# Optimization experiments

Measured on AMD Instinct MI355X. Metric: run time of the kernel, lower is better.

## Reference

```python
import jax, jax.numpy as jnp
import numpy as np

B, L, D, H, DFF = 8, 1024, 256, 8, 2048
DH = D // H


def setup_inputs() -> dict:
    key = jax.random.key(0)
    ks = jax.random.split(key, 12)

    def w(k, shape):
        return jax.random.normal(k, shape, dtype=jnp.float32) * 0.02

    # continuous padding: first `length` tokens valid, rest padded (mask True = pad)
    lengths = jax.random.randint(ks[0], (B,), L // 4, L + 1)
    mask = jnp.arange(L)[None, :] >= lengths[:, None]

    return {
        "src": jax.random.normal(ks[1], (B, L, D), dtype=jnp.float32),
        "src_key_padding_mask": mask,
        "in_proj_w": w(ks[2], (3 * D, D)),
        "in_proj_b": w(ks[3], (3 * D,)),
        "out_w": w(ks[4], (D, D)),
        "out_b": w(ks[5], (D,)),
        "proj_w": w(ks[6], (D, D)),
        "proj_b": w(ks[7], (D,)),
        "ff1_w": w(ks[8], (DFF, D)),
        "ff1_b": w(ks[9], (DFF,)),
        "ff2_w": w(ks[10], (D, DFF)),
        "ff2_b": w(ks[11], (D,)),
    }


def reference(src, src_key_padding_mask, in_proj_w, in_proj_b, out_w, out_b,
              proj_w, proj_b, ff1_w, ff1_b, ff2_w, ff2_b):
    mask = src_key_padding_mask  # [B, L], True = padding
    neg_inf = jnp.float32(-jnp.inf)

    # --- make_attn_mask (vectorized, continuous padding) ---
    s = (~mask).sum(axis=1).astype(jnp.float32)              # [B] valid lengths
    idx = jnp.arange(L, dtype=jnp.float32)
    dist = jnp.abs(idx[:, None] - idx[None, :])              # [L, L]
    valid_tok = idx[None, :] < s[:, None]                    # [B, L]
    pair_ok = valid_tok[:, :, None] & valid_tok[:, None, :]  # [B, L, L]
    bias = jnp.where(pair_ok, (s[:, None, None] - dist[None]) / s[:, None, None], neg_inf)
    # rows that are entirely -inf (padded query rows) are zeroed, like masked_fill
    row_pad = ~valid_tok                                     # [B, L]
    bias = jnp.where(row_pad[:, :, None], 0.0, bias)
    # key_padding_mask is merged additively (as in nn.MultiheadAttention)
    add_mask = bias + jnp.where(mask[:, None, :], neg_inf, 0.0)  # [B, L, L]

    # --- multi-head self-attention ---
    qkv = src @ in_proj_w.T + in_proj_b                      # [B, L, 3D]
    q, k, v = jnp.split(qkv, 3, axis=-1)

    def heads(t):
        return t.reshape(B, L, H, DH).transpose(0, 2, 1, 3)  # [B, H, L, DH]

    q, k, v = heads(q), heads(k), heads(v)
    scale = 1.0 / jnp.sqrt(jnp.float32(DH))
    scores = jnp.einsum('bhqd,bhkd->bhqk', q, k) * scale + add_mask[:, None]
    attn = jax.nn.softmax(scores, axis=-1)
    ctx = jnp.einsum('bhqk,bhkd->bhqd', attn, v)
    ctx = ctx.transpose(0, 2, 1, 3).reshape(B, L, D)
    h_attn = ctx @ out_w.T + out_b

    # --- residual proj + FFN (no layernorm, no dropout) ---
    h = src + (h_attn @ proj_w.T + proj_b)
    ff = jax.nn.gelu(h @ ff1_w.T + ff1_b, approximate=False) @ ff2_w.T + ff2_b
    h = h + ff

    # zero out padded rows (masked_fill with all_neg_inf)
    h = jnp.where(row_pad[:, :, None], 0.0, h)
    return h
```

## Files before the change

### kernel.cpp

```cpp
#include <hip/hip_runtime.h>
#include <hip/hip_bf16.h>


#define BB   8
#define LL   1024
#define DD   256
#define HHN  8
#define DHH  32
#define DFFN 2048

typedef __attribute__((ext_vector_type(8))) __bf16 bf16x8;
typedef __attribute__((ext_vector_type(4))) float f32x4;

__device__ inline void gload16(const void* g, void* l) {
  __builtin_amdgcn_global_load_lds(
      (const __attribute__((address_space(1))) void*)g,
      (__attribute__((address_space(3))) void*)l, 16, 0, 0);
}

#define NCVT0 (BB * LL * DD)
#define NCVT1 (768 * DD)
#define NCVT2 (DFFN * DD)
#define NCVT3 (DD * DFFN)
#define NB_CVT ((NCVT0 + NCVT1 + NCVT2 + NCVT3) / 2048)

__global__ __launch_bounds__(256) void preamble_kernel(
    const float* __restrict__ src, const unsigned char* __restrict__ mb,
    const float* __restrict__ in_proj_w, const float* __restrict__ ff1_w,
    const float* __restrict__ ff2_w, const float* __restrict__ proj_w,
    const float* __restrict__ out_w, const float* __restrict__ proj_b,
    const float* __restrict__ out_b, __hip_bfloat16* __restrict__ src_bf,
    __hip_bfloat16* __restrict__ wqkv_bf, __hip_bfloat16* __restrict__ wff1_bf,
    __hip_bfloat16* __restrict__ wff2_bf, __hip_bfloat16* __restrict__ wc_bf,
    float* __restrict__ bc, int* __restrict__ lens) {
  const int bid = blockIdx.x;
  const int tid = threadIdx.x;
  __shared__ float red[256];
  __shared__ int cnt[BB];
  __shared__ int flag3f, flagNA;

  if (bid < NB_CVT) {
    int i = bid * 2048 + tid * 8;
    const float* s;
    __hip_bfloat16* d;
    if (i < NCVT0) { s = src; d = src_bf; }
    else if (i < NCVT0 + NCVT1) { s = in_proj_w; d = wqkv_bf; i -= NCVT0; }
    else if (i < NCVT0 + NCVT1 + NCVT2) { s = ff1_w; d = wff1_bf; i -= NCVT0 + NCVT1; }
    else { s = ff2_w; d = wff2_bf; i -= NCVT0 + NCVT1 + NCVT2; }
    const float4 a = *(const float4*)(s + i);
    const float4 b = *(const float4*)(s + i + 4);
    bf16x8 o;
    o[0] = (__bf16)a.x; o[1] = (__bf16)a.y; o[2] = (__bf16)a.z; o[3] = (__bf16)a.w;
    o[4] = (__bf16)b.x; o[5] = (__bf16)b.y; o[6] = (__bf16)b.z; o[7] = (__bf16)b.w;
    *(bf16x8*)(d + i) = o;
  } else if (bid == NB_CVT) {
    if (tid == 0) { flag3f = 0; flagNA = 0; }
    if (tid < BB) cnt[tid] = 0;
    __syncthreads();
    for (int i = tid; i < BB * LL; i += 256) {
      unsigned char v = mb[i];
      if (v) {
        if ((i & 3) == 3 && v == 0x3F) flag3f = 1;
        else if (i & 3) flagNA = 1;
      }
    }
    __syncthreads();
    const bool isfloat = (flag3f != 0);
    const bool isbool = (!isfloat) && (flagNA != 0);
    if (isbool) {
      for (int i = tid; i < BB * LL; i += 256)
        if (mb[i] == 0) atomicAdd(&cnt[i >> 10], 1);
    } else {
      const int* mi = (const int*)mb;
      for (int i = tid; i < BB * LL; i += 256)
        if (mi[i] == 0) atomicAdd(&cnt[i >> 10], 1);
    }
    __syncthreads();
    if (tid < BB) lens[tid] = cnt[tid];
  } else {
    const int i0 = (bid - NB_CVT - 1) << 2;
    const int k = tid;
    float acc[4] = {0.f, 0.f, 0.f, 0.f};
    for (int n = 0; n < DD; ++n) {
      const float won = out_w[n * DD + k];
#pragma unroll
      for (int j = 0; j < 4; ++j)
        acc[j] = fmaf(proj_w[(i0 + j) * DD + n], won, acc[j]);
    }
#pragma unroll
    for (int j = 0; j < 4; ++j) wc_bf[(i0 + j) * DD + k] = (__hip_bfloat16)acc[j];
#pragma unroll
    for (int j = 0; j < 4; ++j) {
      red[k] = proj_w[(i0 + j) * DD + k] * out_b[k];
      __syncthreads();
      for (int sft = 128; sft > 0; sft >>= 1) {
        if (k < sft) red[k] += red[k + sft];
        __syncthreads();
      }
      if (k == 0) bc[i0 + j] = proj_b[i0 + j] + red[0];
      __syncthreads();
    }
  }
}

template <int EPI, int BM>
__global__ __launch_bounds__(256) void gemm_bf16(
    const __hip_bfloat16* __restrict__ A, const __hip_bfloat16* __restrict__ W,
    const float* __restrict__ bias, const float* __restrict__ resid,
    float* __restrict__ Cf, __hip_bfloat16* __restrict__ Cb, const int M,
    const int N, const int K, const int* __restrict__ lens) {
  constexpr int MF = BM / 32;
  constexpr int CH = BM / 64;
  __shared__ __bf16 As[2][BM][32];
  __shared__ __bf16 Bs[2][128][32];

  const int tid = threadIdx.x;
  const int w = tid >> 6;
  const int lane = tid & 63;
  const int c = lane & 15;
  const int hq = lane >> 4;
  const int h8 = hq << 3;
  const int wr = w >> 1, wc = w & 1;
  const int c0 = blockIdx.x << 7;
  const int r0 = blockIdx.y * BM;

  const int mylen = lens[r0 >> 10];
  if ((r0 & (LL - 1)) >= mylen) return;

  const int srow = tid >> 2;
  const int scol = (tid & 3) << 3;

  auto STAGE = [&](int buf, int kt) {
    const int k0 = kt << 5;
#pragma unroll
    for (int ch = 0; ch < CH; ++ch)
      gload16(A + (size_t)(r0 + (ch << 6) + srow) * K + k0 + scol,
              &As[buf][(ch << 6) + (w << 4)][0]);
#pragma unroll
    for (int ch = 0; ch < 2; ++ch)
      gload16(W + (size_t)(c0 + (ch << 6) + srow) * K + k0 + scol,
              &Bs[buf][(ch << 6) + (w << 4)][0]);
  };

  f32x4 acc[MF][4];
#pragma unroll
  for (int m = 0; m < MF; ++m)
#pragma unroll
    for (int n = 0; n < 4; ++n) acc[m][n] = (f32x4){0.f, 0.f, 0.f, 0.f};

  const int nkt = K >> 5;
  int buf = 0;
  STAGE(0, 0);
  __syncthreads();
  for (int kt = 0; kt < nkt; ++kt) {
    if (kt + 1 < nkt) STAGE(buf ^ 1, kt + 1);
    bf16x8 af[MF], bfr[4];
#pragma unroll
    for (int m = 0; m < MF; ++m)
      af[m] = *(const bf16x8*)&As[buf][wr * (MF * 16) + (m << 4) + c][h8];
#pragma unroll
    for (int n = 0; n < 4; ++n)
      bfr[n] = *(const bf16x8*)&Bs[buf][(wc << 6) + (n << 4) + c][h8];
#pragma unroll
    for (int m = 0; m < MF; ++m)
#pragma unroll
      for (int n = 0; n < 4; ++n)
        acc[m][n] =
            __builtin_amdgcn_mfma_f32_16x16x32_bf16(af[m], bfr[n], acc[m][n], 0, 0, 0);
    __syncthreads();
    buf ^= 1;
  }

  float bv[4];
#pragma unroll
  for (int n = 0; n < 4; ++n) bv[n] = bias[c0 + (wc << 6) + (n << 4) + c];

#pragma unroll
  for (int m = 0; m < MF; ++m) {
#pragma unroll
    for (int i = 0; i < 4; ++i) {
      const int gr = r0 + wr * (MF * 16) + (m << 4) + (hq << 2) + i;
#pragma unroll
      for (int n = 0; n < 4; ++n) {
        const int gc = c0 + (wc << 6) + (n << 4) + c;
        float v = acc[m][n][i] + bv[n];
        if (EPI == 1) v = 0.5f * v * (1.0f + erff(v * 0.70710678118654752f));
        if (EPI == 2) {
          v += resid[(size_t)gr * N + gc];
          Cf[(size_t)gr * N + gc] = v;
        }
        Cb[(size_t)gr * N + gc] = (__hip_bfloat16)v;
      }
    }
  }
}

__global__ __launch_bounds__(256) void gemm_ff2_part(
    const __hip_bfloat16* __restrict__ A, const __hip_bfloat16* __restrict__ W,
    float* __restrict__ P, const int* __restrict__ lens) {
  constexpr int MF = 2;
  __shared__ __bf16 As[2][64][32];
  __shared__ __bf16 Bs[2][128][32];

  const int tid = threadIdx.x;
  const int w = tid >> 6;
  const int lane = tid & 63;
  const int c = lane & 15;
  const int hq = lane >> 4;
  const int h8 = hq << 3;
  const int wr = w >> 1, wc = w & 1;
  const int c0 = blockIdx.x << 7;
  const int r0 = blockIdx.y << 6;
  if ((r0 & (LL - 1)) >= lens[r0 >> 10]) return;

  const int kz = blockIdx.z;
  const int kbase = kz << 9;
  const int srow = tid >> 2;
  const int scol = (tid & 3) << 3;

  auto STAGE = [&](int buf, int kt) {
    const int k0 = kbase + (kt << 5);
    gload16(A + (size_t)(r0 + srow) * DFFN + k0 + scol, &As[buf][w << 4][0]);
#pragma unroll
    for (int ch = 0; ch < 2; ++ch)
      gload16(W + (size_t)(c0 + (ch << 6) + srow) * DFFN + k0 + scol,
              &Bs[buf][(ch << 6) + (w << 4)][0]);
  };

  f32x4 acc[MF][4];
#pragma unroll
  for (int m = 0; m < MF; ++m)
#pragma unroll
    for (int n = 0; n < 4; ++n) acc[m][n] = (f32x4){0.f, 0.f, 0.f, 0.f};

  int buf = 0;
  STAGE(0, 0);
  __syncthreads();
  for (int kt = 0; kt < 16; ++kt) {
    if (kt + 1 < 16) STAGE(buf ^ 1, kt + 1);
    bf16x8 af[MF], bfr[4];
#pragma unroll
    for (int m = 0; m < MF; ++m)
      af[m] = *(const bf16x8*)&As[buf][wr * (MF * 16) + (m << 4) + c][h8];
#pragma unroll
    for (int n = 0; n < 4; ++n)
      bfr[n] = *(const bf16x8*)&Bs[buf][(wc << 6) + (n << 4) + c][h8];
#pragma unroll
    for (int m = 0; m < MF; ++m)
#pragma unroll
      for (int n = 0; n < 4; ++n)
        acc[m][n] =
            __builtin_amdgcn_mfma_f32_16x16x32_bf16(af[m], bfr[n], acc[m][n], 0, 0, 0);
    __syncthreads();
    buf ^= 1;
  }

  float* Pz = P + (size_t)kz * (BB * LL) * DD;
#pragma unroll
  for (int m = 0; m < MF; ++m)
#pragma unroll
    for (int i = 0; i < 4; ++i) {
      const int gr = r0 + wr * (MF * 16) + (m << 4) + (hq << 2) + i;
#pragma unroll
      for (int n = 0; n < 4; ++n)
        Pz[(size_t)gr * DD + c0 + (wc << 6) + (n << 4) + c] = acc[m][n][i];
    }
}

__global__ __launch_bounds__(256) void ff2_reduce(
    const float* __restrict__ P, const float* __restrict__ resid,
    const float* __restrict__ bias, float* __restrict__ out,
    const int* __restrict__ lens) {
  const int idx = blockIdx.x * 256 + threadIdx.x;
  const int r = idx >> 6;
  const int c4 = (idx & 63) << 2;
  float4 o;
  if ((r & (LL - 1)) >= lens[r >> 10]) {
    o.x = o.y = o.z = o.w = 0.f;
  } else {
    const size_t base = (size_t)r * DD + c4;
    o = *(const float4*)&resid[base];
    const float4 bv = *(const float4*)&bias[c4];
    o.x += bv.x; o.y += bv.y; o.z += bv.z; o.w += bv.w;
#pragma unroll
    for (int z = 0; z < 4; ++z) {
      const float4 pv = *(const float4*)&P[(size_t)z * (BB * LL) * DD + base];
      o.x += pv.x; o.y += pv.y; o.z += pv.z; o.w += pv.w;
    }
  }
  *(float4*)&out[(size_t)r * DD + c4] = o;
}

__global__ __launch_bounds__(256) void attn_fwd_mfma(
    const __hip_bfloat16* __restrict__ qkv, __hip_bfloat16* __restrict__ ctx,
    const int* __restrict__ lens) {
  __shared__ __bf16 Ks[2][64][56];
  __shared__ __bf16 Vt[2][32][66];
  __shared__ __bf16 Pl[4][16][72];

  const int tid = threadIdx.x;
  const int q0 = blockIdx.x << 6;
  const int hh = blockIdx.y;
  const int b = blockIdx.z;
  const int slen = lens[b];
  if (q0 >= slen) return;

  const int w = tid >> 6;
  const int lane = tid & 63;
  const int c = lane & 15;
  const int h = lane >> 4;
  const int h8 = h << 3;

  const float L2E = 1.44269504f;
  const float sf = (float)slen;
  const float cb = -7.0f * L2E;
  const float cd = (1.0f / sf) * L2E;
  const float qscale = 0.17677669529663689f * L2E;

  bf16x8 qf;
  {
    const int qrow = q0 + (w << 4) + c;
    const bf16x8 qraw =
        *(const bf16x8*)(qkv + (size_t)(b * LL + qrow) * 768 + hh * DHH + h8);
#pragma unroll
    for (int j = 0; j < 8; ++j) qf[j] = (__bf16)((float)qraw[j] * qscale);
  }

  f32x4 acc0 = {0.f, 0.f, 0.f, 0.f};
  f32x4 acc1 = {0.f, 0.f, 0.f, 0.f};
  float lsum[4] = {0.f, 0.f, 0.f, 0.f};

  const int skey = tid >> 2;
  const int sdg = (tid & 3) << 3;
  const int ntk = (slen + 63) >> 6;
  const int qg = q0 + (w << 4) + (h << 2);

  const __hip_bfloat16* kvbase = qkv + (size_t)b * LL * 768 + 256 + hh * DHH + sdg;

  bf16x8 kreg, vreg;
  {
    const __hip_bfloat16* kb = kvbase + (size_t)skey * 768;
    kreg = *(const bf16x8*)kb;
    vreg = *(const bf16x8*)(kb + 256);
    *(bf16x8*)&Ks[0][skey][sdg] = kreg;
#pragma unroll
    for (int j = 0; j < 8; ++j) Vt[0][sdg + j][skey] = vreg[j];
  }
  if (ntk > 1) {
    const __hip_bfloat16* kb = kvbase + (size_t)(64 + skey) * 768;
    kreg = *(const bf16x8*)kb;
    vreg = *(const bf16x8*)(kb + 256);
  }
  __syncthreads();

  for (int kt = 0; kt < ntk; ++kt) {
    const int p = kt & 1;
    const int kbase = kt << 6;

    f32x4 st[4];
    __builtin_amdgcn_s_setprio(1);
#pragma unroll
    for (int t = 0; t < 4; ++t) {
      const bf16x8 kf = *(const bf16x8*)&Ks[p][(t << 4) + c][h8];
      st[t] = __builtin_amdgcn_mfma_f32_16x16x32_bf16(
          qf, kf, (f32x4){0.f, 0.f, 0.f, 0.f}, 0, 0, 0);
    }
    __builtin_amdgcn_s_setprio(0);

#pragma unroll
    for (int t = 0; t < 4; ++t) {
      const int kj = kbase + (t << 4) + c;
      const bool kvalid = kj < slen;
      const float kjf = (float)kj;
#pragma unroll
      for (int i = 0; i < 4; ++i) {
        const float dist = fabsf((float)(qg + i) - kjf);
        const float arg = kvalid ? (st[t][i] + cb - dist * cd) : -1e30f;
        const float pv = __builtin_amdgcn_exp2f(arg);
        lsum[i] += pv;
        Pl[w][(h << 2) + i][c + (t << 4)] = (__bf16)pv;
      }
    }

    asm volatile("s_waitcnt lgkmcnt(0)" ::: "memory");

    __builtin_amdgcn_s_setprio(1);
#pragma unroll
    for (int n = 0; n < 2; ++n) {
      const bf16x8 pf = *(const bf16x8*)&Pl[w][c][h8 + (n << 5)];
      const uint32_t* v0p = (const uint32_t*)&Vt[p][c][h8 + (n << 5)];
      const uint32_t* v1p = (const uint32_t*)&Vt[p][16 + c][h8 + (n << 5)];
      union { uint32_t u[4]; bf16x8 v; } t0, t1;
#pragma unroll
      for (int j = 0; j < 4; ++j) { t0.u[j] = v0p[j]; t1.u[j] = v1p[j]; }
      acc0 = __builtin_amdgcn_mfma_f32_16x16x32_bf16(pf, t0.v, acc0, 0, 0, 0);
      acc1 = __builtin_amdgcn_mfma_f32_16x16x32_bf16(pf, t1.v, acc1, 0, 0, 0);
    }
    __builtin_amdgcn_s_setprio(0);

    if (kt + 1 < ntk) {
      *(bf16x8*)&Ks[p ^ 1][skey][sdg] = kreg;
#pragma unroll
      for (int j = 0; j < 8; ++j) Vt[p ^ 1][sdg + j][skey] = vreg[j];
      if (kt + 2 < ntk) {
        const __hip_bfloat16* kb = kvbase + (size_t)(((kt + 2) << 6) + skey) * 768;
        kreg = *(const bf16x8*)kb;
        vreg = *(const bf16x8*)(kb + 256);
      }
    }
    __syncthreads();
  }

#pragma unroll
  for (int i = 0; i < 4; ++i) {
    float l = lsum[i];
    l += __shfl_xor(l, 1);
    l += __shfl_xor(l, 2);
    l += __shfl_xor(l, 4);
    l += __shfl_xor(l, 8);
    const float il = 1.0f / l;
    __hip_bfloat16* op =
        ctx + (size_t)(b * LL + q0 + (w << 4) + (h << 2) + i) * 256 + hh * DHH;
    op[c] = (__hip_bfloat16)(acc0[i] * il);
    op[c + 16] = (__hip_bfloat16)(acc1[i] * il);
  }
}

extern "C" void kernel_launch(void* const* d_in, const int* in_sizes, int n_in,
                              void* d_out, int out_size, void* d_ws,
                              size_t ws_size, hipStream_t stream) {
  (void)in_sizes; (void)n_in; (void)out_size; (void)ws_size;
  const float* src = (const float*)d_in[0];
  const unsigned char* mask = (const unsigned char*)d_in[1];
  const float* in_proj_w = (const float*)d_in[2];
  const float* in_proj_b = (const float*)d_in[3];
  const float* out_w = (const float*)d_in[4];
  const float* out_b = (const float*)d_in[5];
  const float* proj_w = (const float*)d_in[6];
  const float* proj_b = (const float*)d_in[7];
  const float* ff1_w = (const float*)d_in[8];
  const float* ff1_b = (const float*)d_in[9];
  const float* ff2_w = (const float*)d_in[10];
  const float* ff2_b = (const float*)d_in[11];
  float* out = (float*)d_out;

  const int M = BB * LL;
  char* p = (char*)d_ws;
  __hip_bfloat16* qkv_bf = (__hip_bfloat16*)p; p += (size_t)M * 768 * 2;
  __hip_bfloat16* ctx_bf = (__hip_bfloat16*)p; p += (size_t)M * 256 * 2;
  float* hbuf_f = (float*)p;                   p += (size_t)M * 256 * 4;
  __hip_bfloat16* hbuf_bf = (__hip_bfloat16*)p; p += (size_t)M * 256 * 2;
  __hip_bfloat16* ff1o_bf = (__hip_bfloat16*)p; p += (size_t)M * 2048 * 2;
  __hip_bfloat16* src_bf = (__hip_bfloat16*)p;  p += (size_t)M * 256 * 2;
  __hip_bfloat16* wqkv_bf = (__hip_bfloat16*)p; p += (size_t)768 * 256 * 2;
  __hip_bfloat16* wff1_bf = (__hip_bfloat16*)p; p += (size_t)2048 * 256 * 2;
  __hip_bfloat16* wff2_bf = (__hip_bfloat16*)p; p += (size_t)256 * 2048 * 2;
  __hip_bfloat16* wc_bf = (__hip_bfloat16*)p;   p += (size_t)256 * 256 * 2;
  float* bc = (float*)p;                        p += 256 * 4;
  int* lens = (int*)p;                          p += 256;
  float* pbuf = (float*)p;                      p += (size_t)4 * M * 256 * 4;

  preamble_kernel<<<NB_CVT + 1 + 64, 256, 0, stream>>>(
      src, mask, in_proj_w, ff1_w, ff2_w, proj_w, out_w, proj_b, out_b, src_bf,
      wqkv_bf, wff1_bf, wff2_bf, wc_bf, bc, lens);

  gemm_bf16<0, 128><<<dim3(6, 64), 256, 0, stream>>>(
      src_bf, wqkv_bf, in_proj_b, nullptr, nullptr, qkv_bf, M, 768, 256, lens);
  attn_fwd_mfma<<<dim3(LL / 64, HHN, BB), 256, 0, stream>>>(qkv_bf, ctx_bf, lens);
  gemm_bf16<2, 64><<<dim3(2, 128), 256, 0, stream>>>(
      ctx_bf, wc_bf, bc, src, hbuf_f, hbuf_bf, M, 256, 256, lens);
  gemm_bf16<1, 128><<<dim3(16, 64), 256, 0, stream>>>(
      hbuf_bf, wff1_bf, ff1_b, nullptr, nullptr, ff1o_bf, M, 2048, 256, lens);
  gemm_ff2_part<<<dim3(2, 128, 4), 256, 0, stream>>>(ff1o_bf, wff2_bf, pbuf, lens);
  ff2_reduce<<<M * 256 / 4 / 256, 256, 0, stream>>>(pbuf, hbuf_f, ff2_b, out, lens);
}
```

Baseline: 129.7 us.

## Fuse fp32-to-bf16 conversion into QKV GEMM, store FF2 partials in bf16, fast-path unmasked attention tiles

```diff
diff --git a/kernel.cpp b/kernel.cpp
--- a/kernel.cpp
+++ b/kernel.cpp
@@ -18,19 +18,22 @@
       (__attribute__((address_space(3))) void*)l, 16, 0, 0);
 }
 
-#define NCVT0 (BB * LL * DD)
-#define NCVT1 (768 * DD)
+__device__ inline bf16x8 cvt8(const float4 a, const float4 b) {
+  bf16x8 o;
+  o[0] = (__bf16)a.x; o[1] = (__bf16)a.y; o[2] = (__bf16)a.z; o[3] = (__bf16)a.w;
+  o[4] = (__bf16)b.x; o[5] = (__bf16)b.y; o[6] = (__bf16)b.z; o[7] = (__bf16)b.w;
+  return o;
+}
+
 #define NCVT2 (DFFN * DD)
 #define NCVT3 (DD * DFFN)
-#define NB_CVT ((NCVT0 + NCVT1 + NCVT2 + NCVT3) / 2048)
+#define NB_CVT ((NCVT2 + NCVT3) / 2048)
 
 __global__ __launch_bounds__(256) void preamble_kernel(
-    const float* __restrict__ src, const unsigned char* __restrict__ mb,
-    const float* __restrict__ in_proj_w, const float* __restrict__ ff1_w,
+    const unsigned char* __restrict__ mb, const float* __restrict__ ff1_w,
     const float* __restrict__ ff2_w, const float* __restrict__ proj_w,
     const float* __restrict__ out_w, const float* __restrict__ proj_b,
-    const float* __restrict__ out_b, __hip_bfloat16* __restrict__ src_bf,
-    __hip_bfloat16* __restrict__ wqkv_bf, __hip_bfloat16* __restrict__ wff1_bf,
+    const float* __restrict__ out_b, __hip_bfloat16* __restrict__ wff1_bf,
     __hip_bfloat16* __restrict__ wff2_bf, __hip_bfloat16* __restrict__ wc_bf,
     float* __restrict__ bc, int* __restrict__ lens) {
   const int bid = blockIdx.x;
@@ -43,16 +46,11 @@
     int i = bid * 2048 + tid * 8;
     const float* s;
     __hip_bfloat16* d;
-    if (i < NCVT0) { s = src; d = src_bf; }
-    else if (i < NCVT0 + NCVT1) { s = in_proj_w; d = wqkv_bf; i -= NCVT0; }
-    else if (i < NCVT0 + NCVT1 + NCVT2) { s = ff1_w; d = wff1_bf; i -= NCVT0 + NCVT1; }
-    else { s = ff2_w; d = wff2_bf; i -= NCVT0 + NCVT1 + NCVT2; }
+    if (i < NCVT2) { s = ff1_w; d = wff1_bf; }
+    else { s = ff2_w; d = wff2_bf; i -= NCVT2; }
     const float4 a = *(const float4*)(s + i);
     const float4 b = *(const float4*)(s + i + 4);
-    bf16x8 o;
-    o[0] = (__bf16)a.x; o[1] = (__bf16)a.y; o[2] = (__bf16)a.z; o[3] = (__bf16)a.w;
-    o[4] = (__bf16)b.x; o[5] = (__bf16)b.y; o[6] = (__bf16)b.z; o[7] = (__bf16)b.w;
-    *(bf16x8*)(d + i) = o;
+    *(bf16x8*)(d + i) = cvt8(a, b);
   } else if (bid == NB_CVT) {
     if (tid == 0) { flag3f = 0; flagNA = 0; }
     if (tid < BB) cnt[tid] = 0;
@@ -101,6 +99,93 @@
       __syncthreads();
     }
   }
+}
+
+__global__ __launch_bounds__(256) void gemm_qkv(
+    const float* __restrict__ A, const float* __restrict__ W,
+    const float* __restrict__ bias, __hip_bfloat16* __restrict__ Cb,
+    const int* __restrict__ lens) {
+  __shared__ __bf16 As[2][128][32];
+  __shared__ __bf16 Bs[2][128][32];
+
+  const int tid = threadIdx.x;
+  const int w = tid >> 6;
+  const int lane = tid & 63;
+  const int c = lane & 15;
+  const int hq = lane >> 4;
+  const int h8 = hq << 3;
+  const int wr = w >> 1, wc = w & 1;
+  const int c0 = blockIdx.x << 7;
+  const int r0 = blockIdx.y << 7;
+  if ((r0 & (LL - 1)) >= lens[r0 >> 10]) return;
+
+  const int srow = tid >> 2;
+  const int scol = (tid & 3) << 3;
+
+  float4 ra[2][2], rb[2][2];
+  auto LOADR = [&](int kt) {
+    const int k0 = kt << 5;
+#pragma unroll
+    for (int ch = 0; ch < 2; ++ch) {
+      const float* ap = A + (size_t)(r0 + (ch << 6) + srow) * DD + k0 + scol;
+      ra[ch][0] = *(const float4*)ap;
+      ra[ch][1] = *(const float4*)(ap + 4);
+      const float* wp = W + (size_t)(c0 + (ch << 6) + srow) * DD + k0 + scol;
+      rb[ch][0] = *(const float4*)wp;
+      rb[ch][1] = *(const float4*)(wp + 4);
+    }
+  };
+  auto WRITEL = [&](int buf) {
+#pragma unroll
+    for (int ch = 0; ch < 2; ++ch) {
+      *(bf16x8*)&As[buf][(ch << 6) + srow][scol] = cvt8(ra[ch][0], ra[ch][1]);
+      *(bf16x8*)&Bs[buf][(ch << 6) + srow][scol] = cvt8(rb[ch][0], rb[ch][1]);
+    }
+  };
+
+  f32x4 acc[4][4];
+#pragma unroll
+  for (int m = 0; m < 4; ++m)
+#pragma unroll
+    for (int n = 0; n < 4; ++n) acc[m][n] = (f32x4){0.f, 0.f, 0.f, 0.f};
+
+  int buf = 0;
+  LOADR(0);
+  WRITEL(0);
+  __syncthreads();
+  for (int kt = 0; kt < 8; ++kt) {
+    if (kt + 1 < 8) LOADR(kt + 1);
+    bf16x8 af[4], bfr[4];
+#pragma unroll
+    for (int m = 0; m < 4; ++m)
+      af[m] = *(const bf16x8*)&As[buf][wr * 64 + (m << 4) + c][h8];
+#pragma unroll
+    for (int n = 0; n < 4; ++n)
+      bfr[n] = *(const bf16x8*)&Bs[buf][(wc << 6) + (n << 4) + c][h8];
+#pragma unroll
+    for (int m = 0; m < 4; ++m)
+#pragma unroll
+      for (int n = 0; n < 4; ++n)
+        acc[m][n] =
+            __builtin_amdgcn_mfma_f32_16x16x32_bf16(af[m], bfr[n], acc[m][n], 0, 0, 0);
+    if (kt + 1 < 8) WRITEL(buf ^ 1);
+    __syncthreads();
+    buf ^= 1;
+  }
+
+  float bv[4];
+#pragma unroll
+  for (int n = 0; n < 4; ++n) bv[n] = bias[c0 + (wc << 6) + (n << 4) + c];
+#pragma unroll
+  for (int m = 0; m < 4; ++m)
+#pragma unroll
+    for (int i = 0; i < 4; ++i) {
+      const int gr = r0 + wr * 64 + (m << 4) + (hq << 2) + i;
+#pragma unroll
+      for (int n = 0; n < 4; ++n)
+        Cb[(size_t)gr * 768 + c0 + (wc << 6) + (n << 4) + c] =
+            (__hip_bfloat16)(acc[m][n][i] + bv[n]);
+    }
 }
 
 template <int EPI, int BM>
@@ -123,9 +208,7 @@
   const int wr = w >> 1, wc = w & 1;
   const int c0 = blockIdx.x << 7;
   const int r0 = blockIdx.y * BM;
-
-  const int mylen = lens[r0 >> 10];
-  if ((r0 & (LL - 1)) >= mylen) return;
+  if ((r0 & (LL - 1)) >= lens[r0 >> 10]) return;
 
   const int srow = tid >> 2;
   const int scol = (tid & 3) << 3;
@@ -197,7 +280,7 @@
 
 __global__ __launch_bounds__(256) void gemm_ff2_part(
     const __hip_bfloat16* __restrict__ A, const __hip_bfloat16* __restrict__ W,
-    float* __restrict__ P, const int* __restrict__ lens) {
+    __hip_bfloat16* __restrict__ P, const int* __restrict__ lens) {
   constexpr int MF = 2;
   __shared__ __bf16 As[2][64][32];
   __shared__ __bf16 Bs[2][128][32];
@@ -255,7 +338,7 @@
     buf ^= 1;
   }
 
-  float* Pz = P + (size_t)kz * (BB * LL) * DD;
+  __hip_bfloat16* Pz = P + (size_t)kz * (BB * LL) * DD;
 #pragma unroll
   for (int m = 0; m < MF; ++m)
 #pragma unroll
@@ -263,12 +346,13 @@
       const int gr = r0 + wr * (MF * 16) + (m << 4) + (hq << 2) + i;
 #pragma unroll
       for (int n = 0; n < 4; ++n)
-        Pz[(size_t)gr * DD + c0 + (wc << 6) + (n << 4) + c] = acc[m][n][i];
+        Pz[(size_t)gr * DD + c0 + (wc << 6) + (n << 4) + c] =
+            (__hip_bfloat16)acc[m][n][i];
     }
 }
 
 __global__ __launch_bounds__(256) void ff2_reduce(
-    const float* __restrict__ P, const float* __restrict__ resid,
+    const __hip_bfloat16* __restrict__ P, const float* __restrict__ resid,
     const float* __restrict__ bias, float* __restrict__ out,
     const int* __restrict__ lens) {
   const int idx = blockIdx.x * 256 + threadIdx.x;
@@ -284,8 +368,12 @@
     o.x += bv.x; o.y += bv.y; o.z += bv.z; o.w += bv.w;
 #pragma unroll
     for (int z = 0; z < 4; ++z) {
-      const float4 pv = *(const float4*)&P[(size_t)z * (BB * LL) * DD + base];
-      o.x += pv.x; o.y += pv.y; o.z += pv.z; o.w += pv.w;
+      const __hip_bfloat16* pz = P + (size_t)z * (BB * LL) * DD + base;
+      ushort4 pu = *(const ushort4*)pz;
+      o.x += __bfloat162float(*(const __hip_bfloat16*)&pu.x);
+      o.y += __bfloat162float(*(const __hip_bfloat16*)&pu.y);
+      o.z += __bfloat162float(*(const __hip_bfloat16*)&pu.z);
+      o.w += __bfloat162float(*(const __hip_bfloat16*)&pu.w);
     }
   }
   *(float4*)&out[(size_t)r * DD + c4] = o;
@@ -367,18 +455,32 @@
     }
     __builtin_amdgcn_s_setprio(0);
 
-#pragma unroll
-    for (int t = 0; t < 4; ++t) {
-      const int kj = kbase + (t << 4) + c;
-      const bool kvalid = kj < slen;
-      const float kjf = (float)kj;
-#pragma unroll
-      for (int i = 0; i < 4; ++i) {
-        const float dist = fabsf((float)(qg + i) - kjf);
-        const float arg = kvalid ? (st[t][i] + cb - dist * cd) : -1e30f;
-        const float pv = __builtin_amdgcn_exp2f(arg);
-        lsum[i] += pv;
-        Pl[w][(h << 2) + i][c + (t << 4)] = (__bf16)pv;
+    if (kbase + 64 <= slen) {
+#pragma unroll
+      for (int t = 0; t < 4; ++t) {
+        const float kjf = (float)(kbase + (t << 4) + c);
+#pragma unroll
+        for (int i = 0; i < 4; ++i) {
+          const float dist = fabsf((float)(qg + i) - kjf);
+          const float pv = __builtin_amdgcn_exp2f(st[t][i] + cb - dist * cd);
+          lsum[i] += pv;
+          Pl[w][(h << 2) + i][c + (t << 4)] = (__bf16)pv;
+        }
+      }
+    } else {
+#pragma unroll
+      for (int t = 0; t < 4; ++t) {
+        const int kj = kbase + (t << 4) + c;
+        const bool kvalid = kj < slen;
+        const float kjf = (float)kj;
+#pragma unroll
+        for (int i = 0; i < 4; ++i) {
+          const float dist = fabsf((float)(qg + i) - kjf);
+          const float arg = kvalid ? (st[t][i] + cb - dist * cd) : -1e30f;
+          const float pv = __builtin_amdgcn_exp2f(arg);
+          lsum[i] += pv;
+          Pl[w][(h << 2) + i][c + (t << 4)] = (__bf16)pv;
+        }
       }
     }
 
@@ -448,24 +550,22 @@
   char* p = (char*)d_ws;
   __hip_bfloat16* qkv_bf = (__hip_bfloat16*)p; p += (size_t)M * 768 * 2;
   __hip_bfloat16* ctx_bf = (__hip_bfloat16*)p; p += (size_t)M * 256 * 2;
-  float* hbuf_f = (float*)p;                   p += (size_t)M * 256 * 4;
+  float* hbuf_f = (float*)p;                    p += (size_t)M * 256 * 4;
   __hip_bfloat16* hbuf_bf = (__hip_bfloat16*)p; p += (size_t)M * 256 * 2;
   __hip_bfloat16* ff1o_bf = (__hip_bfloat16*)p; p += (size_t)M * 2048 * 2;
-  __hip_bfloat16* src_bf = (__hip_bfloat16*)p;  p += (size_t)M * 256 * 2;
-  __hip_bfloat16* wqkv_bf = (__hip_bfloat16*)p; p += (size_t)768 * 256 * 2;
   __hip_bfloat16* wff1_bf = (__hip_bfloat16*)p; p += (size_t)2048 * 256 * 2;
   __hip_bfloat16* wff2_bf = (__hip_bfloat16*)p; p += (size_t)256 * 2048 * 2;
   __hip_bfloat16* wc_bf = (__hip_bfloat16*)p;   p += (size_t)256 * 256 * 2;
   float* bc = (float*)p;                        p += 256 * 4;
   int* lens = (int*)p;                          p += 256;
-  float* pbuf = (float*)p;                      p += (size_t)4 * M * 256 * 4;
+  __hip_bfloat16* pbuf = (__hip_bfloat16*)p;    p += (size_t)4 * M * 256 * 2;
 
   preamble_kernel<<<NB_CVT + 1 + 64, 256, 0, stream>>>(
-      src, mask, in_proj_w, ff1_w, ff2_w, proj_w, out_w, proj_b, out_b, src_bf,
-      wqkv_bf, wff1_bf, wff2_bf, wc_bf, bc, lens);
-
-  gemm_bf16<0, 128><<<dim3(6, 64), 256, 0, stream>>>(
-      src_bf, wqkv_bf, in_proj_b, nullptr, nullptr, qkv_bf, M, 768, 256, lens);
+      mask, ff1_w, ff2_w, proj_w, out_w, proj_b, out_b, wff1_bf, wff2_bf,
+      wc_bf, bc, lens);
+
+  gemm_qkv<<<dim3(6, 64), 256, 0, stream>>>(src, in_proj_w, in_proj_b, qkv_bf,
+                                            lens);
   attn_fwd_mfma<<<dim3(LL / 64, HHN, BB), 256, 0, stream>>>(qkv_bf, ctx_bf, lens);
   gemm_bf16<2, 64><<<dim3(2, 128), 256, 0, stream>>>(
       ctx_bf, wc_bf, bc, src, hbuf_f, hbuf_bf, M, 256, 256, lens);
```

Result: faster. 126.3 us (-2.6%).
